# Kernel optimization log

Measured on AMD Instinct MI355X. Metric: run time of the kernel, lower is better.

The kernel has to match this reference:

```python
import jax, jax.numpy as jnp
import numpy as np

N_NODES = 100000
N_EDGES = 1600000
D = 64
N_LAYERS = 3
N_GRAPHS = 16
N_CLASSES = 6
BN_EPS = 1e-5


def setup_inputs() -> dict:
    key = jax.random.key(0)
    ks = jax.random.split(key, 20)
    x = jax.random.normal(ks[0], (N_NODES, D), dtype=jnp.float32)
    edge_index = jax.random.randint(ks[1], (2, N_EDGES), 0, N_NODES, dtype=jnp.int64)
    batch = jnp.sort(jax.random.randint(ks[2], (N_NODES,), 0, N_GRAPHS, dtype=jnp.int64))
    s = 1.0 / np.sqrt(D)
    # stacked per-layer MLP params (all layers have in=out=64)
    W1 = jax.random.uniform(ks[3], (N_LAYERS, D, D), jnp.float32, -s, s)
    b1 = jax.random.uniform(ks[4], (N_LAYERS, D), jnp.float32, -s, s)
    g1 = jax.random.uniform(ks[5], (N_LAYERS, D), jnp.float32, 0.5, 1.5)
    be1 = jax.random.normal(ks[6], (N_LAYERS, D)) * 0.1
    m1 = jax.random.normal(ks[7], (N_LAYERS, D)) * 0.1
    v1 = jax.random.uniform(ks[8], (N_LAYERS, D), jnp.float32, 0.5, 1.5)
    W2 = jax.random.uniform(ks[9], (N_LAYERS, D, D), jnp.float32, -s, s)
    b2 = jax.random.uniform(ks[10], (N_LAYERS, D), jnp.float32, -s, s)
    g2 = jax.random.uniform(ks[11], (N_LAYERS, D), jnp.float32, 0.5, 1.5)
    be2 = jax.random.normal(ks[12], (N_LAYERS, D)) * 0.1
    m2 = jax.random.normal(ks[13], (N_LAYERS, D)) * 0.1
    v2 = jax.random.uniform(ks[14], (N_LAYERS, D), jnp.float32, 0.5, 1.5)
    sc = 1.0 / np.sqrt(D)
    wp = jax.random.uniform(ks[15], (D, N_CLASSES), jnp.float32, -sc, sc)
    bp = jax.random.uniform(ks[16], (N_CLASSES,), jnp.float32, -sc, sc)
    ws = jax.random.uniform(ks[17], (D, N_CLASSES), jnp.float32, -sc, sc)
    bs = jax.random.uniform(ks[18], (N_CLASSES,), jnp.float32, -sc, sc)
    return dict(x=x, edge_index=edge_index, batch=batch,
                W1=W1, b1=b1, g1=g1, be1=be1, m1=m1, v1=v1,
                W2=W2, b2=b2, g2=g2, be2=be2, m2=m2, v2=v2,
                wp=wp, bp=bp, ws=ws, bs=bs)


def _bn(h, gamma, beta, mean, var):
    return (h - mean) * (gamma / jnp.sqrt(var + BN_EPS)) + beta


def reference(x, edge_index, batch, W1, b1, g1, be1, m1, v1,
              W2, b2, g2, be2, m2, v2, wp, bp, ws, bs):
    src, dst = edge_index[0], edge_index[1]
    h = x
    for i in range(N_LAYERS):
        # GINConv (eps=0): (1+eps)*h + sum_{j in N(i)} h_j
        agg = jax.ops.segment_sum(h[src], dst, num_segments=N_NODES)
        z = h + agg
        z = _bn(z @ W1[i] + b1[i], g1[i], be1[i], m1[i], v1[i])
        z = jax.nn.relu(z)
        z = _bn(z @ W2[i] + b2[i], g2[i], be2[i], m2[i], v2[i])
        h = jax.nn.relu(z)  # outer F.relu in forward
    # global mean pool over graphs
    sums = jax.ops.segment_sum(h, batch, num_segments=N_GRAPHS)
    cnts = jax.ops.segment_sum(jnp.ones((h.shape[0],), h.dtype), batch, num_segments=N_GRAPHS)
    pooled = sums / jnp.maximum(cnts, 1.0)[:, None]  # [G, D]
    primary = pooled @ wp + bp
    secondary = pooled @ ws + bs
    return primary, secondary
```

## Files before the change

### kernel.cpp

```cpp
#include <hip/hip_runtime.h>
#include <hip/hip_bf16.h>

#define NCLASSES 6
#define NGRAPHS 16
#define BN_EPS 1e-5f
#define SCAN_BLOCK 256
#define SCAN_ITEMS 16
#define NB2 512

typedef __attribute__((ext_vector_type(8))) short short8v;
typedef __attribute__((ext_vector_type(4))) float float4v;

__device__ __forceinline__ float bf2f(unsigned short u) {
  union { unsigned int i; float f; } v;
  v.i = ((unsigned int)u) << 16;
  return v.f;
}
__device__ __forceinline__ unsigned short f2bf(float f) {
  union { unsigned int i; float f; } v;
  v.f = f;
  unsigned int b = v.i + 0x7FFFu + ((v.i >> 16) & 1u);
  return (unsigned short)(b >> 16);
}

__global__ __launch_bounds__(256) void k_cast(const float* __restrict__ x,
                                              unsigned short* __restrict__ hx,
                                              int total4) {
  int i = blockIdx.x * blockDim.x + threadIdx.x;
  int stride = gridDim.x * blockDim.x;
  for (; i < total4; i += stride) {
    float4 f = reinterpret_cast<const float4*>(x)[i];
    ushort4 o;
    o.x = f2bf(f.x); o.y = f2bf(f.y); o.z = f2bf(f.z); o.w = f2bf(f.w);
    reinterpret_cast<ushort4*>(hx)[i] = o;
  }
}

__global__ void k_fold(const float* __restrict__ W1, const float* __restrict__ b1,
                       const float* __restrict__ g1, const float* __restrict__ be1,
                       const float* __restrict__ m1, const float* __restrict__ v1,
                       const float* __restrict__ W2, const float* __restrict__ b2,
                       const float* __restrict__ g2, const float* __restrict__ be2,
                       const float* __restrict__ m2, const float* __restrict__ v2,
                       unsigned short* __restrict__ Wfb, float* __restrict__ Sf) {
  int idx = blockIdx.x * blockDim.x + threadIdx.x;
  if (idx >= 3 * 2 * 2 * 4 * 64 * 8) return;
  int j = idx & 7;
  int lane = (idx >> 3) & 63;
  int t = (idx >> 9) & 3;
  int h = (idx >> 11) & 1;
  int mat = (idx >> 12) & 1;
  int l = idx >> 13;
  int k = 32 * h + 8 * (lane >> 4) + j;
  int d = 16 * t + (lane & 15);
  const float* W = mat ? W2 : W1;
  const float* b = mat ? b2 : b1;
  const float* g = mat ? g2 : g1;
  const float* be = mat ? be2 : be1;
  const float* m = mat ? m2 : m1;
  const float* v = mat ? v2 : v1;
  float scale = g[l * 64 + d] * rsqrtf(v[l * 64 + d] + BN_EPS);
  Wfb[idx] = f2bf(W[(l * 64 + k) * 64 + d] * scale);
  if (h == 0 && j == 0)
    Sf[(l * 2 + mat) * 64 + d] = be[l * 64 + d] + (b[l * 64 + d] - m[l * 64 + d]) * scale;
}

__global__ __launch_bounds__(256) void k_bcount(const int* __restrict__ dst, int nE,
                                                int chunk, int nbk,
                                                int* __restrict__ hist) {
  __shared__ int lcnt[512];
  for (int i = threadIdx.x; i < nbk; i += 256) lcnt[i] = 0;
  __syncthreads();
  int blk = blockIdx.x;
  int c0 = blk * chunk, c1 = min(nE, c0 + chunk);
  for (int e = c0 + threadIdx.x; e < c1; e += 256) atomicAdd(&lcnt[dst[e] >> 8], 1);
  __syncthreads();
  for (int k = threadIdx.x; k < nbk; k += 256) hist[k * NB2 + blk] = lcnt[k];
}

__global__ __launch_bounds__(SCAN_BLOCK) void k_scan_partial(
    const int* __restrict__ in, int n, int* __restrict__ partials) {
  __shared__ int lds[SCAN_BLOCK];
  int t = threadIdx.x;
  int base = blockIdx.x * SCAN_BLOCK * SCAN_ITEMS + t * SCAN_ITEMS;
  int s = 0;
#pragma unroll
  for (int i = 0; i < SCAN_ITEMS; ++i) {
    int idx = base + i;
    if (idx < n) s += in[idx];
  }
  lds[t] = s;
  __syncthreads();
  for (int off = SCAN_BLOCK / 2; off > 0; off >>= 1) {
    if (t < off) lds[t] += lds[t + off];
    __syncthreads();
  }
  if (t == 0) partials[blockIdx.x] = lds[0];
}

__global__ void k_scan_root(int* __restrict__ partials, int nb) {
  if (threadIdx.x == 0) {
    int run = 0;
    for (int i = 0; i < nb; ++i) {
      int v = partials[i];
      partials[i] = run;
      run += v;
    }
  }
}

__global__ __launch_bounds__(SCAN_BLOCK) void k_scan_write(
    const int* __restrict__ in, int n, const int* __restrict__ partials,
    int* __restrict__ out_excl) {
  __shared__ int lds[SCAN_BLOCK];
  int t = threadIdx.x;
  int base = blockIdx.x * SCAN_BLOCK * SCAN_ITEMS + t * SCAN_ITEMS;
  int local[SCAN_ITEMS];
  int s = 0;
#pragma unroll
  for (int i = 0; i < SCAN_ITEMS; ++i) {
    int idx = base + i;
    int v = (idx < n) ? in[idx] : 0;
    local[i] = v;
    s += v;
  }
  lds[t] = s;
  __syncthreads();
  int val = s;
  for (int off = 1; off < SCAN_BLOCK; off <<= 1) {
    int tmp = (t >= off) ? lds[t - off] : 0;
    __syncthreads();
    val += tmp;
    lds[t] = val;
    __syncthreads();
  }
  int run = partials[blockIdx.x] + val - s;
#pragma unroll
  for (int i = 0; i < SCAN_ITEMS; ++i) {
    int idx = base + i;
    if (idx < n) {
      out_excl[idx] = run;
      run += local[i];
    }
  }
}

__global__ void k_boff(const int* __restrict__ hist_base, int nbk, int nE,
                       int* __restrict__ boff) {
  int t = blockIdx.x * blockDim.x + threadIdx.x;
  if (t < nbk) boff[t] = hist_base[t * NB2];
  if (t == nbk) boff[nbk] = nE;
}

__global__ __launch_bounds__(256) void k_bscatter(const int* __restrict__ src,
                                                  const int* __restrict__ dst, int nE,
                                                  int chunk, int nbk,
                                                  const int* __restrict__ hist_base,
                                                  int* __restrict__ ebuf) {
  __shared__ int cur[512];
  int blk = blockIdx.x;
  for (int k = threadIdx.x; k < nbk; k += 256) cur[k] = hist_base[k * NB2 + blk];
  __syncthreads();
  int c0 = blk * chunk, c1 = min(nE, c0 + chunk);
  for (int e = c0 + threadIdx.x; e < c1; e += 256) {
    int d = dst[e];
    int pos = atomicAdd(&cur[d >> 8], 1);
    ebuf[pos] = (src[e] << 8) | (d & 255);
  }
}

__global__ __launch_bounds__(256) void k_bsort(const int* __restrict__ ebuf,
                                               const int* __restrict__ boff, int nbk,
                                               int n, int nE, int* __restrict__ offs,
                                               int* __restrict__ csr_src) {
  __shared__ int cnt[256], sc[256], cur[256];
  int b = blockIdx.x, t = threadIdx.x;
  int e0 = boff[b], e1 = boff[b + 1];
  int node0 = b << 8;
  cnt[t] = 0;
  __syncthreads();
  for (int e = e0 + t; e < e1; e += 256) atomicAdd(&cnt[ebuf[e] & 255], 1);
  __syncthreads();
  int v = cnt[t];
  sc[t] = v;
  __syncthreads();
  int val = v;
  for (int off = 1; off < 256; off <<= 1) {
    int tmp = (t >= off) ? sc[t - off] : 0;
    __syncthreads();
    val += tmp;
    sc[t] = val;
    __syncthreads();
  }
  int excl = val - v;
  int node = node0 + t;
  if (node < n) offs[node] = e0 + excl;
  cur[t] = e0 + excl;
  if (b == nbk - 1 && t == 0) offs[n] = nE;
  __syncthreads();
  for (int e = e0 + t; e < e1; e += 256) {
    int pr = ebuf[e];
    int pos = atomicAdd(&cur[pr & 255], 1);
    csr_src[pos] = ((unsigned int)pr) >> 8;
  }
}

__global__ __launch_bounds__(256, 8) void k_gather(
    const unsigned short* __restrict__ h_in, unsigned short* __restrict__ z,
    const int* __restrict__ offs, const int* __restrict__ csr_src, int n) {
  const int lane = threadIdx.x & 63;
  int wave = blockIdx.x * 4 + (threadIdx.x >> 6);
  int nwaves = gridDim.x * 4;
  for (int node = wave; node < n; node += nwaves) {
    float acc = bf2f(h_in[(size_t)node * 64 + lane]);
    int e0 = __builtin_amdgcn_readfirstlane(offs[node]);
    int e1 = __builtin_amdgcn_readfirstlane(offs[node + 1]);
    int e = e0;
    float a0 = 0.f, a1 = 0.f, a2 = 0.f, a3 = 0.f;
    float a4 = 0.f, a5 = 0.f, a6 = 0.f, a7 = 0.f;
    for (; e + 7 < e1; e += 8) {
      int q0 = __builtin_amdgcn_readfirstlane(csr_src[e]);
      int q1 = __builtin_amdgcn_readfirstlane(csr_src[e + 1]);
      int q2 = __builtin_amdgcn_readfirstlane(csr_src[e + 2]);
      int q3 = __builtin_amdgcn_readfirstlane(csr_src[e + 3]);
      int q4 = __builtin_amdgcn_readfirstlane(csr_src[e + 4]);
      int q5 = __builtin_amdgcn_readfirstlane(csr_src[e + 5]);
      int q6 = __builtin_amdgcn_readfirstlane(csr_src[e + 6]);
      int q7 = __builtin_amdgcn_readfirstlane(csr_src[e + 7]);
      a0 += bf2f(h_in[(size_t)q0 * 64 + lane]);
      a1 += bf2f(h_in[(size_t)q1 * 64 + lane]);
      a2 += bf2f(h_in[(size_t)q2 * 64 + lane]);
      a3 += bf2f(h_in[(size_t)q3 * 64 + lane]);
      a4 += bf2f(h_in[(size_t)q4 * 64 + lane]);
      a5 += bf2f(h_in[(size_t)q5 * 64 + lane]);
      a6 += bf2f(h_in[(size_t)q6 * 64 + lane]);
      a7 += bf2f(h_in[(size_t)q7 * 64 + lane]);
    }
    for (; e < e1; ++e) {
      int q = __builtin_amdgcn_readfirstlane(csr_src[e]);
      a0 += bf2f(h_in[(size_t)q * 64 + lane]);
    }
    acc += ((a0 + a1) + (a2 + a3)) + ((a4 + a5) + (a6 + a7));
    z[(size_t)node * 64 + lane] = f2bf(acc);
  }
}

__global__ __launch_bounds__(256, 2) void k_mlp(
    const unsigned short* __restrict__ z_in, unsigned short* __restrict__ h_out,
    const unsigned short* __restrict__ Wfb, const float* __restrict__ Sf, int n) {
  __shared__ __align__(16) unsigned short tile[4][16 * 64];
  const int lane = threadIdx.x & 63;
  const int wslot = threadIdx.x >> 6;
  const int g = lane >> 4, c = lane & 15;
  unsigned short* T = tile[wslot];

  const short8v* Wv = reinterpret_cast<const short8v*>(Wfb);
  short8v w1f[4][2], w2f[4][2];
#pragma unroll
  for (int h = 0; h < 2; ++h)
#pragma unroll
    for (int t = 0; t < 4; ++t) {
      w1f[t][h] = Wv[((0 * 2 + h) * 4 + t) * 64 + lane];
      w2f[t][h] = Wv[((1 * 2 + h) * 4 + t) * 64 + lane];
    }
  float s1v[4], s2v[4];
#pragma unroll
  for (int t = 0; t < 4; ++t) {
    s1v[t] = Sf[c + 16 * t];
    s2v[t] = Sf[64 + c + 16 * t];
  }

  int wave = blockIdx.x * 4 + wslot;
  int nwaves = gridDim.x * 4;
  int ntiles = (n + 15) >> 4;
  for (int tt = wave; tt < ntiles; tt += nwaves) {
    int node0 = tt << 4;
    int arow = node0 + c;
    if (arow >= n) arow = n - 1;
    const short8v* zrow = reinterpret_cast<const short8v*>(z_in + (size_t)arow * 64);
    short8v a0 = zrow[g];
    short8v a1 = zrow[g + 4];

    float4v c1[4];
#pragma unroll
    for (int t = 0; t < 4; ++t) {
      float4v acc = {s1v[t], s1v[t], s1v[t], s1v[t]};
      acc = __builtin_amdgcn_mfma_f32_16x16x32_bf16(a0, w1f[t][0], acc, 0, 0, 0);
      acc = __builtin_amdgcn_mfma_f32_16x16x32_bf16(a1, w1f[t][1], acc, 0, 0, 0);
      c1[t] = acc;
    }

#pragma unroll
    for (int t = 0; t < 4; ++t)
#pragma unroll
      for (int r = 0; r < 4; ++r) {
        int m = 4 * g + r;
        int byte = ((c + 16 * t) * 2) ^ ((m & 7) << 4);
        T[(m * 128 + byte) >> 1] = f2bf(fmaxf(c1[t][r], 0.f));
      }
    asm volatile("s_waitcnt lgkmcnt(0)" ::: "memory");
    __builtin_amdgcn_sched_barrier(0);

    int rb = c * 128;
    int sw = (c & 7) << 4;
    short8v a20 = *reinterpret_cast<const short8v*>(&T[(rb + ((g * 16) ^ sw)) >> 1]);
    short8v a21 = *reinterpret_cast<const short8v*>(&T[(rb + ((64 + g * 16) ^ sw)) >> 1]);
    asm volatile("s_waitcnt lgkmcnt(0)" ::: "memory");
    __builtin_amdgcn_sched_barrier(0);

    float4v c2[4];
#pragma unroll
    for (int t = 0; t < 4; ++t) {
      float4v acc = {s2v[t], s2v[t], s2v[t], s2v[t]};
      acc = __builtin_amdgcn_mfma_f32_16x16x32_bf16(a20, w2f[t][0], acc, 0, 0, 0);
      acc = __builtin_amdgcn_mfma_f32_16x16x32_bf16(a21, w2f[t][1], acc, 0, 0, 0);
      c2[t] = acc;
    }

#pragma unroll
    for (int t = 0; t < 4; ++t)
#pragma unroll
      for (int r = 0; r < 4; ++r) {
        int m = 4 * g + r;
        int byte = ((c + 16 * t) * 2) ^ ((m & 7) << 4);
        T[(m * 128 + byte) >> 1] = f2bf(fmaxf(c2[t][r], 0.f));
      }
    asm volatile("s_waitcnt lgkmcnt(0)" ::: "memory");
    __builtin_amdgcn_sched_barrier(0);

    {
      int rho = lane >> 2;
      int node = node0 + rho;
      if (node < n) {
        int cb = (lane & 3) * 32;
        int swr = (rho & 7) << 4;
        short8v v0 = *reinterpret_cast<const short8v*>(&T[(rho * 128 + (cb ^ swr)) >> 1]);
        short8v v1 =
            *reinterpret_cast<const short8v*>(&T[(rho * 128 + ((cb + 16) ^ swr)) >> 1]);
        short8v* orow = reinterpret_cast<short8v*>(h_out + (size_t)node * 64);
        orow[(lane & 3) * 2] = v0;
        orow[(lane & 3) * 2 + 1] = v1;
      }
    }
    asm volatile("s_waitcnt lgkmcnt(0)" ::: "memory");
    __builtin_amdgcn_sched_barrier(0);
  }
}

__global__ __launch_bounds__(256) void k_pool(const unsigned short* __restrict__ h,
                                              const int* __restrict__ batch, int n,
                                              float* __restrict__ gsum,
                                              float* __restrict__ gcnt) {
  __shared__ float lsum[NGRAPHS * 64];
  __shared__ float lcnt[NGRAPHS];
  for (int i = threadIdx.x; i < NGRAPHS * 64; i += 256) lsum[i] = 0.f;
  if (threadIdx.x < NGRAPHS) lcnt[threadIdx.x] = 0.f;
  __syncthreads();
  int lane = threadIdx.x & 63, wslot = threadIdx.x >> 6;
  int wave = blockIdx.x * 4 + wslot, nw = gridDim.x * 4;
  for (int node = wave; node < n; node += nw) {
    int g = batch[node];
    atomicAdd(&lsum[g * 64 + lane], bf2f(h[(size_t)node * 64 + lane]));
    if (lane == 0) atomicAdd(&lcnt[g], 1.f);
  }
  __syncthreads();
  for (int i = threadIdx.x; i < NGRAPHS * 64; i += 256) atomicAdd(&gsum[i], lsum[i]);
  if (threadIdx.x < NGRAPHS) atomicAdd(&gcnt[threadIdx.x], lcnt[threadIdx.x]);
}

__global__ void k_head(const float* __restrict__ gsum, const float* __restrict__ gcnt,
                       const float* __restrict__ wp, const float* __restrict__ bp,
                       const float* __restrict__ wsec, const float* __restrict__ bsec,
                       float* __restrict__ out) {
  int t = threadIdx.x;
  if (t >= NGRAPHS * NCLASSES) return;
  int g = t / NCLASSES, c = t % NCLASSES;
  float inv = 1.f / fmaxf(gcnt[g], 1.f);
  float p = 0.f, s = 0.f;
  for (int d = 0; d < 64; ++d) {
    float pd = gsum[g * 64 + d] * inv;
    p = fmaf(pd, wp[d * NCLASSES + c], p);
    s = fmaf(pd, wsec[d * NCLASSES + c], s);
  }
  out[t] = p + bp[c];
  out[NGRAPHS * NCLASSES + t] = s + bsec[c];
}

extern "C" void kernel_launch(void* const* d_in, const int* in_sizes, int n_in,
                              void* d_out, int out_size, void* d_ws, size_t ws_size,
                              hipStream_t stream) {
  const float* x = (const float*)d_in[0];
  const int* ei = (const int*)d_in[1];
  const int* batch = (const int*)d_in[2];
  const float* W1 = (const float*)d_in[3];
  const float* b1 = (const float*)d_in[4];
  const float* g1 = (const float*)d_in[5];
  const float* be1 = (const float*)d_in[6];
  const float* m1 = (const float*)d_in[7];
  const float* v1 = (const float*)d_in[8];
  const float* W2 = (const float*)d_in[9];
  const float* b2 = (const float*)d_in[10];
  const float* g2 = (const float*)d_in[11];
  const float* be2 = (const float*)d_in[12];
  const float* m2 = (const float*)d_in[13];
  const float* v2 = (const float*)d_in[14];
  const float* wp = (const float*)d_in[15];
  const float* bp = (const float*)d_in[16];
  const float* wsec = (const float*)d_in[17];
  const float* bsec = (const float*)d_in[18];

  const int nE = in_sizes[1] / 2;
  const int n = in_sizes[0] / 64;
  const int NBK = (n + 255) >> 8;
  const int chunk = (nE + NB2 - 1) / NB2;

  char* p = (char*)d_ws;
  auto alloc = [&](size_t bytes) {
    char* r = p;
    p += (bytes + 255) & ~(size_t)255;
    return r;
  };
  unsigned short* hx = (unsigned short*)alloc((size_t)n * 64 * 2);
  unsigned short* hA = (unsigned short*)alloc((size_t)n * 64 * 2);
  unsigned short* hB = (unsigned short*)alloc((size_t)n * 64 * 2);
  unsigned short* zbuf = (unsigned short*)alloc((size_t)n * 64 * 2);
  int* csr = (int*)alloc((size_t)nE * 4);
  int* offs = (int*)alloc((size_t)(n + 1) * 4);
  int* hist = (int*)alloc((size_t)NBK * NB2 * 4);
  int* hist_base = (int*)alloc((size_t)NBK * NB2 * 4);
  int* boff = (int*)alloc((size_t)(NBK + 1) * 4);
  int* partials = (int*)alloc(1024 * 4);
  unsigned short* Wfb = (unsigned short*)alloc(3 * 2 * 2 * 4 * 64 * 8 * 2);
  float* Sf = (float*)alloc(3 * 2 * 64 * 4);
  float* gsum = (float*)alloc(NGRAPHS * 64 * 4);
  float* gcnt = (float*)alloc(NGRAPHS * 4);
  int* ebuf = (int*)zbuf;

  const int* srcA = ei;
  const int* dstA = ei + nE;

  hipMemsetAsync(gsum, 0, NGRAPHS * 64 * 4, stream);
  hipMemsetAsync(gcnt, 0, NGRAPHS * 4, stream);

  k_cast<<<1024, 256, 0, stream>>>(x, hx, n * 64 / 4);
  k_fold<<<96, 256, 0, stream>>>(W1, b1, g1, be1, m1, v1, W2, b2, g2, be2, m2, v2,
                                 Wfb, Sf);

  k_bcount<<<NB2, 256, 0, stream>>>(dstA, nE, chunk, NBK, hist);
  const int ns = NBK * NB2;
  const int nbs = (ns + SCAN_BLOCK * SCAN_ITEMS - 1) / (SCAN_BLOCK * SCAN_ITEMS);
  k_scan_partial<<<nbs, SCAN_BLOCK, 0, stream>>>(hist, ns, partials);
  k_scan_root<<<1, 64, 0, stream>>>(partials, nbs);
  k_scan_write<<<nbs, SCAN_BLOCK, 0, stream>>>(hist, ns, partials, hist_base);
  k_boff<<<(NBK + 1 + 255) / 256, 256, 0, stream>>>(hist_base, NBK, nE, boff);
  k_bscatter<<<NB2, 256, 0, stream>>>(srcA, dstA, nE, chunk, NBK, hist_base, ebuf);
  k_bsort<<<NBK, 256, 0, stream>>>(ebuf, boff, NBK, n, nE, offs, csr);

  const int GB = 2048;
  const int MB = 512;
  const unsigned short* hin = hx;
  unsigned short* houts[3] = {hA, hB, hA};
  for (int l = 0; l < 3; ++l) {
    k_gather<<<GB, 256, 0, stream>>>(hin, zbuf, offs, csr, n);
    k_mlp<<<MB, 256, 0, stream>>>(zbuf, houts[l], Wfb + l * 8192, Sf + l * 128, n);
    hin = houts[l];
  }

  k_pool<<<512, 256, 0, stream>>>(hA, batch, n, gsum, gcnt);
  k_head<<<1, 128, 0, stream>>>(gsum, gcnt, wp, bp, wsec, bsec, (float*)d_out);
}
```

Before: 373.3 us.

## Pad CSR neighbor lists to multiples of eight with a zero sentinel node

Each node's neighbor list in the CSR is padded up to a multiple of 8 entries, and the padding entries point at an extra all-zero row appended to each feature buffer. This lets the gather kernel drop its scalar remainder loop and always run the 8-way unrolled loop. Building the padded layout needs a second counting pass, a block-level prefix scan and a third kernel, plus a larger CSR array. In exchange, the gather does extra loads of the sentinel row (about 3.5 padding entries per node on average).

Measured after the change: 356.4 us. -4.5%, faster.

```diff
diff --git a/kernel.cpp b/kernel.cpp
--- a/kernel.cpp
+++ b/kernel.cpp
@@ -169,10 +169,50 @@
   }
 }
 
-__global__ __launch_bounds__(256) void k_bsort(const int* __restrict__ ebuf,
-                                               const int* __restrict__ boff, int nbk,
-                                               int n, int nE, int* __restrict__ offs,
-                                               int* __restrict__ csr_src) {
+__global__ __launch_bounds__(256) void k_bsortA(const int* __restrict__ ebuf,
+                                                const int* __restrict__ boff,
+                                                int* __restrict__ pbtot) {
+  __shared__ int cnt[256], red[256];
+  int b = blockIdx.x, t = threadIdx.x;
+  int e0 = boff[b], e1 = boff[b + 1];
+  cnt[t] = 0;
+  __syncthreads();
+  for (int e = e0 + t; e < e1; e += 256) atomicAdd(&cnt[ebuf[e] & 255], 1);
+  __syncthreads();
+  red[t] = (cnt[t] + 7) & ~7;
+  __syncthreads();
+  for (int off = 128; off > 0; off >>= 1) {
+    if (t < off) red[t] += red[t + off];
+    __syncthreads();
+  }
+  if (t == 0) pbtot[b] = red[0];
+}
+
+__global__ __launch_bounds__(512) void k_pscan(const int* __restrict__ pbtot, int nbk,
+                                               int* __restrict__ pbase, int n,
+                                               int* __restrict__ offs) {
+  __shared__ int s[512];
+  int t = threadIdx.x;
+  int v = (t < nbk) ? pbtot[t] : 0;
+  s[t] = v;
+  __syncthreads();
+  int val = v;
+  for (int off = 1; off < 512; off <<= 1) {
+    int tmp = (t >= off) ? s[t - off] : 0;
+    __syncthreads();
+    val += tmp;
+    s[t] = val;
+    __syncthreads();
+  }
+  if (t < nbk) pbase[t] = val - v;
+  if (t == nbk - 1) offs[n] = val;
+}
+
+__global__ __launch_bounds__(256) void k_bsortB(const int* __restrict__ ebuf,
+                                                const int* __restrict__ boff,
+                                                const int* __restrict__ pbase, int n,
+                                                int* __restrict__ offs,
+                                                int* __restrict__ csr_src) {
   __shared__ int cnt[256], sc[256], cur[256];
   int b = blockIdx.x, t = threadIdx.x;
   int e0 = boff[b], e1 = boff[b + 1];
@@ -181,10 +221,11 @@
   __syncthreads();
   for (int e = e0 + t; e < e1; e += 256) atomicAdd(&cnt[ebuf[e] & 255], 1);
   __syncthreads();
-  int v = cnt[t];
-  sc[t] = v;
-  __syncthreads();
-  int val = v;
+  int c = cnt[t];
+  int pc = (c + 7) & ~7;
+  sc[t] = pc;
+  __syncthreads();
+  int val = pc;
   for (int off = 1; off < 256; off <<= 1) {
     int tmp = (t >= off) ? sc[t - off] : 0;
     __syncthreads();
@@ -192,17 +233,18 @@
     sc[t] = val;
     __syncthreads();
   }
-  int excl = val - v;
+  int base = pbase[b] + val - pc;
   int node = node0 + t;
-  if (node < n) offs[node] = e0 + excl;
-  cur[t] = e0 + excl;
-  if (b == nbk - 1 && t == 0) offs[n] = nE;
+  if (node < n) offs[node] = base;
+  cur[t] = base;
   __syncthreads();
   for (int e = e0 + t; e < e1; e += 256) {
     int pr = ebuf[e];
     int pos = atomicAdd(&cur[pr & 255], 1);
     csr_src[pos] = ((unsigned int)pr) >> 8;
   }
+  __syncthreads();
+  for (int i = c; i < pc; ++i) csr_src[base + i] = n;
 }
 
 __global__ __launch_bounds__(256, 8) void k_gather(
@@ -215,10 +257,9 @@
     float acc = bf2f(h_in[(size_t)node * 64 + lane]);
     int e0 = __builtin_amdgcn_readfirstlane(offs[node]);
     int e1 = __builtin_amdgcn_readfirstlane(offs[node + 1]);
-    int e = e0;
     float a0 = 0.f, a1 = 0.f, a2 = 0.f, a3 = 0.f;
     float a4 = 0.f, a5 = 0.f, a6 = 0.f, a7 = 0.f;
-    for (; e + 7 < e1; e += 8) {
+    for (int e = e0; e + 7 < e1; e += 8) {
       int q0 = __builtin_amdgcn_readfirstlane(csr_src[e]);
       int q1 = __builtin_amdgcn_readfirstlane(csr_src[e + 1]);
       int q2 = __builtin_amdgcn_readfirstlane(csr_src[e + 2]);
@@ -235,10 +276,6 @@
       a5 += bf2f(h_in[(size_t)q5 * 64 + lane]);
       a6 += bf2f(h_in[(size_t)q6 * 64 + lane]);
       a7 += bf2f(h_in[(size_t)q7 * 64 + lane]);
-    }
-    for (; e < e1; ++e) {
-      int q = __builtin_amdgcn_readfirstlane(csr_src[e]);
-      a0 += bf2f(h_in[(size_t)q * 64 + lane]);
     }
     acc += ((a0 + a1) + (a2 + a3)) + ((a4 + a5) + (a6 + a7));
     z[(size_t)node * 64 + lane] = f2bf(acc);
@@ -420,16 +457,18 @@
     p += (bytes + 255) & ~(size_t)255;
     return r;
   };
-  unsigned short* hx = (unsigned short*)alloc((size_t)n * 64 * 2);
-  unsigned short* hA = (unsigned short*)alloc((size_t)n * 64 * 2);
-  unsigned short* hB = (unsigned short*)alloc((size_t)n * 64 * 2);
+  unsigned short* hx = (unsigned short*)alloc((size_t)(n + 1) * 64 * 2);
+  unsigned short* hA = (unsigned short*)alloc((size_t)(n + 1) * 64 * 2);
+  unsigned short* hB = (unsigned short*)alloc((size_t)(n + 1) * 64 * 2);
   unsigned short* zbuf = (unsigned short*)alloc((size_t)n * 64 * 2);
-  int* csr = (int*)alloc((size_t)nE * 4);
+  int* csr = (int*)alloc(((size_t)nE + 8 * (size_t)n + 64) * 4);
   int* offs = (int*)alloc((size_t)(n + 1) * 4);
   int* hist = (int*)alloc((size_t)NBK * NB2 * 4);
   int* hist_base = (int*)alloc((size_t)NBK * NB2 * 4);
   int* boff = (int*)alloc((size_t)(NBK + 1) * 4);
   int* partials = (int*)alloc(1024 * 4);
+  int* pbtot = (int*)alloc(512 * 4);
+  int* pbase = (int*)alloc(512 * 4);
   unsigned short* Wfb = (unsigned short*)alloc(3 * 2 * 2 * 4 * 64 * 8 * 2);
   float* Sf = (float*)alloc(3 * 2 * 64 * 4);
   float* gsum = (float*)alloc(NGRAPHS * 64 * 4);
@@ -441,6 +480,9 @@
 
   hipMemsetAsync(gsum, 0, NGRAPHS * 64 * 4, stream);
   hipMemsetAsync(gcnt, 0, NGRAPHS * 4, stream);
+  hipMemsetAsync(hx + (size_t)n * 64, 0, 128, stream);
+  hipMemsetAsync(hA + (size_t)n * 64, 0, 128, stream);
+  hipMemsetAsync(hB + (size_t)n * 64, 0, 128, stream);
 
   k_cast<<<1024, 256, 0, stream>>>(x, hx, n * 64 / 4);
   k_fold<<<96, 256, 0, stream>>>(W1, b1, g1, be1, m1, v1, W2, b2, g2, be2, m2, v2,
@@ -454,7 +496,9 @@
   k_scan_write<<<nbs, SCAN_BLOCK, 0, stream>>>(hist, ns, partials, hist_base);
   k_boff<<<(NBK + 1 + 255) / 256, 256, 0, stream>>>(hist_base, NBK, nE, boff);
   k_bscatter<<<NB2, 256, 0, stream>>>(srcA, dstA, nE, chunk, NBK, hist_base, ebuf);
-  k_bsort<<<NBK, 256, 0, stream>>>(ebuf, boff, NBK, n, nE, offs, csr);
+  k_bsortA<<<NBK, 256, 0, stream>>>(ebuf, boff, pbtot);
+  k_pscan<<<1, 512, 0, stream>>>(pbtot, NBK, pbase, n, offs);
+  k_bsortB<<<NBK, 256, 0, stream>>>(ebuf, boff, pbase, n, offs, csr);
 
   const int GB = 2048;
   const int MB = 512;
```
